# Kernel optimization log

Measured on AMD Instinct MI355X. Metric: run time of the kernel, lower is better.

Reference implementation:

```python
import jax, jax.numpy as jnp
import numpy as np

EPS = 1e-5

def conv2d(x, w, pad):
    # x: NCHW, w: OIHW, stride 1, symmetric padding
    return jax.lax.conv_general_dilated(
        x, w, window_strides=(1, 1), padding=[(pad, pad), (pad, pad)],
        dimension_numbers=('NCHW', 'OIHW', 'NCHW'))

def bn_eval(x, gamma, beta, mean, var):
    # eval-mode BatchNorm2d: per-channel affine with running stats
    s = gamma / jnp.sqrt(var + EPS)
    return x * s[None, :, None, None] + (beta - mean * s)[None, :, None, None]

def setup_inputs() -> dict:
    key = jax.random.key(0)
    ks = jax.random.split(key, 12)
    B, Cin, C, H, W = 2, 6, 64, 512, 512
    R, K = 4, 5                 # res_num, ksize
    Cf = 2 * 3 * K              # ch_out_final = 30
    d = {}
    d['feature_map'] = jax.random.normal(ks[0], (B, Cin, H, W), jnp.float32)
    d['base'] = jax.random.normal(ks[1], (B, 3, H, W), jnp.float32)
    d['w_first'] = jax.random.normal(ks[2], (C, Cin, 7, 7), jnp.float32) * 0.05
    d['kb_w1'] = jax.random.normal(ks[3], (R, C, C, 3, 3), jnp.float32) * 0.05
    d['kb_g1'] = jnp.ones((R, C), jnp.float32)
    d['kb_b1'] = jnp.zeros((R, C), jnp.float32)
    d['kb_m1'] = jax.random.normal(ks[4], (R, C), jnp.float32) * 0.1
    d['kb_v1'] = jax.random.uniform(ks[5], (R, C), jnp.float32) + 0.5
    d['kb_w2'] = jax.random.normal(ks[6], (R, C, C, 3, 3), jnp.float32) * 0.05
    d['kb_g2'] = jnp.ones((R, C), jnp.float32)
    d['kb_b2'] = jnp.zeros((R, C), jnp.float32)
    d['kb_m2'] = jax.random.normal(ks[7], (R, C), jnp.float32) * 0.1
    d['kb_v2'] = jax.random.uniform(ks[8], (R, C), jnp.float32) + 0.5
    d['w_last'] = jax.random.normal(ks[9], (Cf, C, 3, 3), jnp.float32) * 0.05
    return d

def reference(feature_map, base, w_first, kb_w1, kb_g1, kb_b1, kb_m1, kb_v1,
              kb_w2, kb_g2, kb_b2, kb_m2, kb_v2, w_last):
    K = 5
    P = K // 2
    b, _, h, w = base.shape
    # conv_first: 7x7 conv + ReLU
    y = jax.nn.relu(conv2d(feature_map, w_first, 3))
    # residual KB blocks: (conv3x3 -> BN -> ReLU) x2 + skip
    R = kb_w1.shape[0]
    for i in range(R):
        t = jax.nn.relu(bn_eval(conv2d(y, kb_w1[i], 1), kb_g1[i], kb_b1[i], kb_m1[i], kb_v1[i]))
        t = jax.nn.relu(bn_eval(conv2d(t, kb_w2[i], 1), kb_g2[i], kb_b2[i], kb_m2[i], kb_v2[i]))
        y = t + y
    # conv_last: [b, 2*3*K, h, w]
    y = conv2d(y, w_last, 1)
    Cf = y.shape[1]
    # [b,3,2K,h,w] -> [b,3,h,w,2K]
    weight = y.reshape(b, 3, Cf // 3, h, w).transpose(0, 1, 3, 4, 2)
    weight_h = jax.nn.softmax(weight[..., :K], axis=-1)  # [b,3,h,w,K]
    weight_w = jax.nn.softmax(weight[..., K:], axis=-1)
    # vertical adaptive filtering: pad H by P, unfold along H
    pad_h = jnp.pad(base, ((0, 0), (0, 0), (P, P), (0, 0)))
    unf_h = jnp.stack([pad_h[:, :, i:i + h, :] for i in range(K)], axis=-1)  # [b,3,h,w,K]
    filt_h = (unf_h * weight_h).sum(axis=-1)  # [b,3,h,w]
    # horizontal adaptive filtering: pad W by P, unfold along W
    pad_w = jnp.pad(filt_h, ((0, 0), (0, 0), (0, 0), (P, P)))
    unf_w = jnp.stack([pad_w[:, :, :, i:i + w] for i in range(K)], axis=-1)  # [b,3,h,w,K]
    return (unf_w * weight_w).sum(axis=-1)
```

## Files before the change

kernel.cpp:

```cpp
#include <hip/hip_runtime.h>
#include <math.h>

typedef __attribute__((ext_vector_type(8)))  short short8;
typedef __attribute__((ext_vector_type(4)))  float float4v;
typedef __attribute__((ext_vector_type(16))) float f32x16;
typedef unsigned int u32;

__device__ __forceinline__ unsigned short f2bf(float f) {
    union { float f; unsigned u; } x; x.f = f;
    unsigned r = x.u + 0x7FFFu + ((x.u >> 16) & 1u);
    return (unsigned short)(r >> 16);
}
__device__ __forceinline__ float bf2f(unsigned short u) {
    union { unsigned u; float f; } x; x.u = ((unsigned)u) << 16;
    return x.f;
}

__device__ __forceinline__ void gload16(const void* g, void* l) {
    __builtin_amdgcn_global_load_lds(
        (const __attribute__((address_space(1))) u32*)g,
        (__attribute__((address_space(3))) u32*)l, 16, 0, 0);
}

#define HWSZ ((size_t)512 * 512)

__global__ __launch_bounds__(256)
void prep7_k(const float* __restrict__ in, unsigned short* __restrict__ hi,
             unsigned short* __restrict__ lo)
{
    const int idx = blockIdx.x * 256 + threadIdx.x;
    const int b = idx >> 18, rem = idx & 262143;
    const int h = rem >> 9, w = rem & 511;
    unsigned short vh[8], vl[8];
#pragma unroll
    for (int c = 0; c < 8; ++c) {
        float x = (c < 6) ? in[((size_t)(b * 6 + c)) * HWSZ + (h << 9) + w] : 0.f;
        unsigned short h16 = f2bf(x);
        vh[c] = h16;
        vl[c] = f2bf(x - bf2f(h16));
    }
    const size_t o = ((size_t)idx) * 8;
    *(uint4*)(hi + o) = *(uint4*)vh;
    *(uint4*)(lo + o) = *(uint4*)vl;
}

__global__ __launch_bounds__(256)
void repack7_k(const float* __restrict__ wsrc, unsigned short* __restrict__ dhi,
               unsigned short* __restrict__ dlo)
{
    const int t = blockIdx.x * 256 + threadIdx.x;
    if (t >= 26624) return;
    const int j = t & 7, l = (t >> 3) & 63, ct = (t >> 9) & 3, kk = t >> 11;
    const int co = ct * 16 + (l & 15);
    const int s = kk * 4 + (l >> 4);
    float v = 0.f;
    if (s < 49 && j < 6)
        v = wsrc[((size_t)(co * 6 + j) * 7 + s / 7) * 7 + s % 7];
    unsigned short h16 = f2bf(v);
    dhi[t] = h16;
    dlo[t] = f2bf(v - bf2f(h16));
}

__global__ __launch_bounds__(256)
void conv7_mfma(const unsigned short* __restrict__ inhi,
                const unsigned short* __restrict__ inlo,
                const unsigned short* __restrict__ whi,
                const unsigned short* __restrict__ wlo,
                unsigned short* __restrict__ out)
{
    extern __shared__ char p_lds[];

    const int id = blockIdx.x;
    const int lid = (id & 7) * 256 + (id >> 3);
    const int w0 = (lid & 3) * 128;
    const int rest = lid >> 2;
    const int h0 = (rest & 255) * 2;
    const int b  = rest >> 8;

    const int tid = threadIdx.x;
    const int wv = tid >> 6, l = tid & 63, lq = l >> 4, lr = l & 15;

    for (int idx = tid; idx < 2144; idx += 256) {
        const int plane = idx >= 1072;
        const int rc = plane ? idx - 1072 : idx;
        const int r = rc / 134, c = rc % 134;
        const int hh = h0 - 3 + r, wc = w0 - 3 + c;
        int4 v = make_int4(0, 0, 0, 0);
        if (hh >= 0 && hh < 512 && wc >= 0 && wc < 512) {
            const unsigned short* src = plane ? inlo : inhi;
            v = *(const int4*)(src + ((((size_t)b * 512 + hh) * 512) + wc) * 8);
        }
        *(int4*)(p_lds + (size_t)idx * 16) = v;
    }
    __syncthreads();

    float4v acc[2][2][4];
#pragma unroll
    for (int pr = 0; pr < 2; ++pr)
#pragma unroll
        for (int pb = 0; pb < 2; ++pb)
#pragma unroll
            for (int ct = 0; ct < 4; ++ct)
                acc[pr][pb][ct] = (float4v){0.f, 0.f, 0.f, 0.f};

    const int cbase = wv * 32 + lr;
#pragma unroll
    for (int kk = 0; kk < 13; ++kk) {
        int s = kk * 4 + lq;
        if (s > 48) s = 48;
        const int dh = s / 7, dwd = s % 7;
        short8 ah[2][2], al[2][2];
#pragma unroll
        for (int pr = 0; pr < 2; ++pr)
#pragma unroll
            for (int pb = 0; pb < 2; ++pb) {
                const int off = ((pr + dh) * 134 + cbase + pb * 16 + dwd) * 16;
                ah[pr][pb] = *(const short8*)(p_lds + off);
                al[pr][pb] = *(const short8*)(p_lds + 17152 + off);
            }
#pragma unroll
        for (int ct = 0; ct < 4; ++ct) {
            const short8 bh = *(const short8*)(whi + ((size_t)(kk * 4 + ct) * 64 + l) * 8);
            const short8 bl = *(const short8*)(wlo + ((size_t)(kk * 4 + ct) * 64 + l) * 8);
#pragma unroll
            for (int pr = 0; pr < 2; ++pr)
#pragma unroll
                for (int pb = 0; pb < 2; ++pb) {
                    acc[pr][pb][ct] = __builtin_amdgcn_mfma_f32_16x16x32_bf16(ah[pr][pb], bh, acc[pr][pb][ct], 0, 0, 0);
                    acc[pr][pb][ct] = __builtin_amdgcn_mfma_f32_16x16x32_bf16(al[pr][pb], bh, acc[pr][pb][ct], 0, 0, 0);
                    acc[pr][pb][ct] = __builtin_amdgcn_mfma_f32_16x16x32_bf16(ah[pr][pb], bl, acc[pr][pb][ct], 0, 0, 0);
                }
        }
    }

#pragma unroll
    for (int pr = 0; pr < 2; ++pr) {
        const int h = h0 + pr;
#pragma unroll
        for (int pb = 0; pb < 2; ++pb) {
            const int col0 = w0 + wv * 32 + pb * 16 + lq * 4;
#pragma unroll
            for (int ct = 0; ct < 4; ++ct) {
                const int half = ct >> 1, colocal = (ct & 1) * 16 + lr;
#pragma unroll
                for (int rg = 0; rg < 4; ++rg) {
                    const size_t o = ((((size_t)(b * 2 + half) * 512 + h) * 512) + (col0 + rg)) * 32 + colocal;
                    out[o] = f2bf(fmaxf(acc[pr][pb][ct][rg], 0.f));
                }
            }
        }
    }
}

__global__ __launch_bounds__(256)
void repack3n_k(const float* __restrict__ w1, const float* __restrict__ w2,
                const float* __restrict__ g1, const float* __restrict__ v1,
                const float* __restrict__ g2, const float* __restrict__ v2,
                unsigned short* __restrict__ dst)
{
    const int conv = blockIdx.z;
    const float* src = (conv < 4) ? (w1 + (size_t)conv * 36864) : (w2 + (size_t)(conv - 4) * 36864);
    const float* g = (conv < 4) ? (g1 + conv * 64) : (g2 + (conv - 4) * 64);
    const float* vv = (conv < 4) ? (v1 + conv * 64) : (v2 + (conv - 4) * 64);
    unsigned short* d = dst + (size_t)conv * 36864;

    const int t = blockIdx.x * 256 + threadIdx.x;
    const int j = t & 7, l = (t >> 3) & 63;
    const int rest = t >> 9;
    const int s = rest % 9, m = rest / 9;
    const int ch = m & 1, q = m >> 1;
    const int co = ch * 32 + (l & 31);
    const int ci = q * 16 + (l >> 5) * 8 + j;
    const float sc = g[co] * rsqrtf(vv[co] + 1e-5f);
    d[t] = f2bf(src[((size_t)co * 64 + ci) * 9 + s] * sc);
}

__global__ __launch_bounds__(256)
void bias8_k(const float* __restrict__ g1, const float* __restrict__ b1,
             const float* __restrict__ m1, const float* __restrict__ v1,
             const float* __restrict__ g2, const float* __restrict__ b2,
             const float* __restrict__ m2, const float* __restrict__ v2,
             float* __restrict__ bias)
{
    const int t = blockIdx.x * 256 + threadIdx.x;
    if (t >= 512) return;
    const int conv = t >> 6, co = t & 63;
    const float* g = (conv < 4) ? (g1 + conv * 64) : (g2 + (conv - 4) * 64);
    const float* be = (conv < 4) ? (b1 + conv * 64) : (b2 + (conv - 4) * 64);
    const float* mn = (conv < 4) ? (m1 + conv * 64) : (m2 + (conv - 4) * 64);
    const float* vv = (conv < 4) ? (v1 + conv * 64) : (v2 + (conv - 4) * 64);
    const float sc = g[co] * rsqrtf(vv[co] + 1e-5f);
    bias[t] = be[co] - mn[co] * sc;
}

template <bool ADD_>
__global__ __launch_bounds__(512)
void conv3_mfma32(const unsigned short* __restrict__ in,
                  const unsigned short* __restrict__ wrp,
                  const float* __restrict__ bias,
                  const unsigned short* __restrict__ skip,
                  unsigned short* __restrict__ out)
{
    extern __shared__ char smem[];
    char* w_lds = smem;
    char* p_lds = smem + 18432;

    const int id = blockIdx.x;
    const int lid = (id & 7) * 128 + (id >> 3);
    const int w0 = (lid & 3) * 128;
    const int h0 = ((lid >> 2) & 127) * 4;
    const int b  = lid >> 9;

    const int tid = threadIdx.x;
    const int wv = tid >> 6, l = tid & 63;
    const int rw = wv >> 1, tq = wv & 1;
    const int lo5 = l & 31, hi = l >> 5;

    f32x16 acc[2][2];
#pragma unroll
    for (int ch = 0; ch < 2; ++ch)
#pragma unroll
        for (int t4 = 0; t4 < 2; ++t4)
#pragma unroll
            for (int e = 0; e < 16; ++e) acc[ch][t4][e] = 0.f;

    for (int q = 0; q < 4; ++q) {
        if (q) __syncthreads();

        const unsigned short* wq  = wrp + (size_t)q * 9216;
        const unsigned short* inp = in + (size_t)(b * 2 + (q >> 1)) * HWSZ * 32;
        const int cb8 = (q & 1) * 2;

        for (int i = wv; i < 42; i += 8) {
            if (i < 18) {
                gload16(wq + (size_t)i * 512 + l * 8, w_lds + (size_t)i * 1024);
            } else {
                const int j2 = i - 18, p = j2 >> 1, half = j2 & 1;
                const int row = p >> 1, kg = p & 1;
                const int hh = h0 - 1 + row;
                if (hh >= 0 && hh < 512)
                    gload16(inp + ((size_t)hh * 512 + w0 + half * 64 + l) * 32 + (cb8 + kg) * 8,
                            p_lds + (size_t)(p * 132 + 1 + half * 64) * 16);
            }
        }
        if (tid < 24) {
            const int p = tid >> 1, side = tid & 1;
            const int row = p >> 1, kg = p & 1;
            const int hh = h0 - 1 + row;
            const int wc = side ? (w0 + 128) : (w0 - 1);
            int4 v = make_int4(0, 0, 0, 0);
            if (hh >= 0 && hh < 512 && wc >= 0 && wc < 512)
                v = *(const int4*)(inp + ((size_t)hh * 512 + wc) * 32 + (cb8 + kg) * 8);
            *(int4*)(p_lds + (size_t)(p * 132 + (side ? 129 : 0)) * 16) = v;
        }
        if (h0 == 0) {
            for (int g = tid; g < 264; g += 512)
                *(int4*)(p_lds + (size_t)g * 16) = make_int4(0, 0, 0, 0);
        } else if (h0 == 508) {
            for (int g = tid; g < 264; g += 512)
                *(int4*)(p_lds + (size_t)(10 * 132 + g) * 16) = make_int4(0, 0, 0, 0);
        }
        __syncthreads();

#pragma unroll
        for (int s = 0; s < 9; ++s) {
            const int dh = s / 3, dwd = s % 3;
            const int row = rw + dh;
            short8 pf[2];
#pragma unroll
            for (int t4 = 0; t4 < 2; ++t4) {
                const int px = tq * 64 + t4 * 32 + dwd + lo5;
                pf[t4] = *(const short8*)(p_lds +
                    ((size_t)((row * 2 + hi) * 132 + px)) * 16);
            }
#pragma unroll
            for (int ch = 0; ch < 2; ++ch) {
                const short8 w8 = *(const short8*)(w_lds +
                    ((size_t)((ch * 9 + s) * 64 + l)) * 16);
#pragma unroll
                for (int t4 = 0; t4 < 2; ++t4)
                    acc[ch][t4] = __builtin_amdgcn_mfma_f32_32x32x16_bf16(
                        pf[t4], w8, acc[ch][t4], 0, 0, 0);
            }
        }
    }

    const int h = h0 + rw;
#pragma unroll
    for (int ch = 0; ch < 2; ++ch) {
        const float bvs = bias[ch * 32 + lo5];
        const size_t pbase = ((size_t)(b * 2 + ch) * HWSZ + (size_t)h * 512);
#pragma unroll
        for (int t4 = 0; t4 < 2; ++t4) {
#pragma unroll
            for (int reg = 0; reg < 16; ++reg) {
                const int pxl = tq * 64 + t4 * 32 + (reg & 3) + 8 * (reg >> 2) + 4 * hi;
                const size_t o = (pbase + (w0 + pxl)) * 32 + lo5;
                float v = fmaxf(acc[ch][t4][reg] + bvs, 0.f);
                if (ADD_) v += bf2f(skip[o]);
                out[o] = f2bf(v);
            }
        }
    }
}

__global__ __launch_bounds__(256)
void repackL_k(const float* __restrict__ wsrc, unsigned short* __restrict__ d)
{
    const int t = blockIdx.x * 256 + threadIdx.x;
    const int j = t & 7, l = (t >> 3) & 63, ct = (t >> 9) & 1, kks = t >> 10;
    const int hf = kks / 9, s = kks % 9;
    const int co = ct * 16 + (l & 15);
    const int ci = hf * 32 + (l >> 4) * 8 + j;
    d[t] = (co < 30) ? f2bf(wsrc[((size_t)co * 64 + ci) * 9 + s]) : (unsigned short)0;
}

template <int NCOT, int OC>
__global__ __launch_bounds__(256)
void conv3_last(const unsigned short* __restrict__ in,
                const unsigned short* __restrict__ wrp,
                unsigned short* __restrict__ out)
{
    extern __shared__ char smem[];
    unsigned short* w_lds = (unsigned short*)smem;
    char* p_lds = smem + NCOT * 9 * 1024;

    const int id = blockIdx.x;
    const int lid = (id & 7) * 256 + (id >> 3);
    const int w0 = (lid & 3) * 128;
    const int rest = lid >> 2;
    const int h0 = (rest & 255) * 2;
    const int b  = rest >> 8;

    const int tid = threadIdx.x;
    const int wv = tid >> 6, l = tid & 63, lq = l >> 4, lr = l & 15;
    const int cbase = wv * 32 + lr;

    float4v acc[2][2][NCOT];
#pragma unroll
    for (int pr = 0; pr < 2; ++pr)
#pragma unroll
        for (int pb = 0; pb < 2; ++pb)
#pragma unroll
            for (int ct = 0; ct < NCOT; ++ct)
                acc[pr][pb][ct] = (float4v){0.f, 0.f, 0.f, 0.f};

    for (int ph = 0; ph < 2; ++ph) {
        const int4* wsrc = (const int4*)(wrp + (size_t)ph * 9 * NCOT * 512);
        for (int i = tid; i < NCOT * 9 * 64; i += 256)
            ((int4*)w_lds)[i] = wsrc[i];
        const unsigned short* inp = in + (size_t)(b * 2 + ph) * HWSZ * 32;
        for (int idx = tid; idx < 2080; idx += 256) {
            const int G = idx & 3, c = (idx >> 2) % 130, rr = idx / 520;
            const int hh = h0 - 1 + rr, wc = w0 - 1 + c;
            int4 v = make_int4(0, 0, 0, 0);
            if (hh >= 0 && hh < 512 && wc >= 0 && wc < 512)
                v = *(const int4*)(inp + ((size_t)hh * 512 + wc) * 32 + G * 8);
            *(int4*)(p_lds + ((size_t)(G * 521 + rr * 130 + c)) * 16) = v;
        }
        __syncthreads();

#pragma unroll
        for (int s = 0; s < 9; ++s) {
            const int dh = s / 3, dwd = s % 3;
            short8 a[2][2];
#pragma unroll
            for (int pr = 0; pr < 2; ++pr)
#pragma unroll
                for (int pb = 0; pb < 2; ++pb)
                    a[pr][pb] = *(const short8*)(p_lds +
                        ((size_t)(lq * 521 + (pr + dh) * 130 + cbase + pb * 16 + dwd)) * 16);
#pragma unroll
            for (int ct = 0; ct < NCOT; ++ct) {
                const short8 bw = *(const short8*)(w_lds + ((size_t)(s * NCOT + ct) * 64 + l) * 8);
#pragma unroll
                for (int pr = 0; pr < 2; ++pr)
#pragma unroll
                    for (int pb = 0; pb < 2; ++pb)
                        acc[pr][pb][ct] = __builtin_amdgcn_mfma_f32_16x16x32_bf16(
                            a[pr][pb], bw, acc[pr][pb][ct], 0, 0, 0);
            }
        }
        __syncthreads();
    }

#pragma unroll
    for (int pr = 0; pr < 2; ++pr) {
        const int h = h0 + pr;
#pragma unroll
        for (int pb = 0; pb < 2; ++pb) {
            const int col0 = w0 + wv * 32 + pb * 16 + lq * 4;
#pragma unroll
            for (int ct = 0; ct < NCOT; ++ct) {
                const int co = ct * 16 + lr;
                if (co < OC) {
#pragma unroll
                    for (int rg = 0; rg < 4; ++rg) {
                        const size_t o = (((size_t)(b * OC + co) * 512 + h) * 512) + (col0 + rg);
                        out[o] = f2bf(acc[pr][pb][ct][rg]);
                    }
                }
            }
        }
    }
}

__global__ __launch_bounds__(256)
void filt_fused_k(const unsigned short* __restrict__ wl, const float* __restrict__ base,
                  float* __restrict__ out)
{
    __shared__ float F[516];

    const int id = blockIdx.x;
    const int lid = (id & 7) * 384 + (id >> 3);
    const int h = lid & 511;
    const int bc = lid >> 9;
    const int b = bc / 3, c = bc % 3;
    const int t = threadIdx.x;

    if (t < 2) F[t] = 0.f;
    if (t >= 254) F[t + 260] = 0.f;

    const size_t rowoff = (size_t)h * 512;
    const unsigned short* wv_p = wl + ((size_t)(b * 30 + c * 10) * HWSZ) + rowoff;
    const unsigned short* wh_p = wv_p + 5 * HWSZ;
    const float* bp = base + (size_t)bc * HWSZ;

#pragma unroll
    for (int wi = 0; wi < 2; ++wi) {
        const int w = t + wi * 256;
        float v[5]; float mx = -1e30f;
#pragma unroll
        for (int i = 0; i < 5; ++i) { v[i] = bf2f(wv_p[(size_t)i * HWSZ + w]); mx = fmaxf(mx, v[i]); }
        float sm = 0.f;
#pragma unroll
        for (int i = 0; i < 5; ++i) { v[i] = __expf(v[i] - mx); sm += v[i]; }
        const float inv = 1.f / sm;
        float acc = 0.f;
#pragma unroll
        for (int i = 0; i < 5; ++i) {
            const int hh = h + i - 2;
            const float bvv = (hh >= 0 && hh < 512) ? bp[(size_t)hh * 512 + w] : 0.f;
            acc = fmaf(bvv, v[i] * inv, acc);
        }
        F[w + 2] = acc;
    }
    __syncthreads();

#pragma unroll
    for (int wi = 0; wi < 2; ++wi) {
        const int w = t + wi * 256;
        float v[5]; float mx = -1e30f;
#pragma unroll
        for (int i = 0; i < 5; ++i) { v[i] = bf2f(wh_p[(size_t)i * HWSZ + w]); mx = fmaxf(mx, v[i]); }
        float sm = 0.f;
#pragma unroll
        for (int i = 0; i < 5; ++i) { v[i] = __expf(v[i] - mx); sm += v[i]; }
        const float inv = 1.f / sm;
        float acc = 0.f;
#pragma unroll
        for (int i = 0; i < 5; ++i)
            acc = fmaf(F[w + i], v[i] * inv, acc);
        out[(size_t)bc * HWSZ + rowoff + w] = acc;
    }
}

extern "C" void kernel_launch(void* const* d_in, const int* in_sizes, int n_in,
                              void* d_out, int out_size, void* d_ws, size_t ws_size,
                              hipStream_t stream)
{
    const float* fm      = (const float*)d_in[0];
    const float* base    = (const float*)d_in[1];
    const float* w_first = (const float*)d_in[2];
    const float* kb_w1   = (const float*)d_in[3];
    const float* kb_g1   = (const float*)d_in[4];
    const float* kb_b1   = (const float*)d_in[5];
    const float* kb_m1   = (const float*)d_in[6];
    const float* kb_v1   = (const float*)d_in[7];
    const float* kb_w2   = (const float*)d_in[8];
    const float* kb_g2   = (const float*)d_in[9];
    const float* kb_b2   = (const float*)d_in[10];
    const float* kb_m2   = (const float*)d_in[11];
    const float* kb_v2   = (const float*)d_in[12];
    const float* w_last  = (const float*)d_in[13];

    char* ws = (char*)d_ws;
    unsigned short* wrp3n  = (unsigned short*)ws;
    unsigned short* wrpL   = wrp3n + (size_t)8 * 36864;
    unsigned short* wrp7hi = wrpL + 18432;
    unsigned short* wrp7lo = wrp7hi + 26624;
    float*          biasws = (float*)(wrp7lo + 26624);
    unsigned short* actA = (unsigned short*)(ws + (1 << 20));
    unsigned short* actB = actA + (size_t)2 * HWSZ * 64;
    unsigned short* actC = actB + (size_t)2 * HWSZ * 64;
    unsigned short* in7hi = actB;
    unsigned short* in7lo = actB + (size_t)2 * HWSZ * 8;
    unsigned short* logits = actC;

    hipFuncSetAttribute((const void*)conv3_mfma32<false>,
                        hipFuncAttributeMaxDynamicSharedMemorySize, 43776);
    hipFuncSetAttribute((const void*)conv3_mfma32<true>,
                        hipFuncAttributeMaxDynamicSharedMemorySize, 43776);
    hipFuncSetAttribute((const void*)conv3_last<2, 30>,
                        hipFuncAttributeMaxDynamicSharedMemorySize, 51776);
    hipFuncSetAttribute((const void*)conv7_mfma,
                        hipFuncAttributeMaxDynamicSharedMemorySize, 34304);

    dim3 blk(256);

    repack3n_k<<<dim3(144, 1, 8), blk, 0, stream>>>(kb_w1, kb_w2, kb_g1, kb_v1, kb_g2, kb_v2, wrp3n);
    bias8_k<<<dim3(2, 1, 1), blk, 0, stream>>>(kb_g1, kb_b1, kb_m1, kb_v1, kb_g2, kb_b2, kb_m2, kb_v2, biasws);
    repackL_k<<<dim3(72, 1, 1), blk, 0, stream>>>(w_last, wrpL);
    repack7_k<<<dim3(104, 1, 1), blk, 0, stream>>>(w_first, wrp7hi, wrp7lo);
    prep7_k<<<dim3(2048, 1, 1), blk, 0, stream>>>(fm, in7hi, in7lo);

    conv7_mfma<<<dim3(2048, 1, 1), blk, 34304, stream>>>(in7hi, in7lo, wrp7hi, wrp7lo, actA);

    unsigned short* cur = actA;
    unsigned short* oth = actC;
    for (int i = 0; i < 4; ++i) {
        conv3_mfma32<false><<<dim3(1024, 1, 1), dim3(512), 43776, stream>>>(
            cur, wrp3n + (size_t)i * 36864, biasws + i * 64, nullptr, actB);
        conv3_mfma32<true><<<dim3(1024, 1, 1), dim3(512), 43776, stream>>>(
            actB, wrp3n + (size_t)(4 + i) * 36864, biasws + (4 + i) * 64, cur, oth);
        unsigned short* t = cur; cur = oth; oth = t;
    }

    conv3_last<2, 30><<<dim3(2048, 1, 1), blk, 51776, stream>>>(cur, wrpL, logits);

    filt_fused_k<<<dim3(3072, 1, 1), blk, 0, stream>>>(logits, base, (float*)d_out);
}
```

Baseline: 552.5 us.

## Rewrite last conv with 32x32x16 MFMA, weight-stationary tiling and async LDS loads

Replaces the final 64->30 3x3 conv kernel with one that uses 32x32x16 bf16 MFMA, putting the 32 padded output channels on the A side and pixels on the B side. The weight repack layout changes to match. All weights are loaded once via global_load_lds, and the input tile is staged in four channel-quarter passes using direct-to-LDS loads plus explicit halo and boundary zeroing. The aim is fewer MFMA issues, less register-level shuffling and cheaper LDS staging, at the cost of more barriers and more shared memory per block.

```diff
diff --git a/kernel.cpp b/kernel.cpp
--- a/kernel.cpp
+++ b/kernel.cpp
@@ -305,102 +305,103 @@
 }
 
 __global__ __launch_bounds__(256)
-void repackL_k(const float* __restrict__ wsrc, unsigned short* __restrict__ d)
+void repackLn_k(const float* __restrict__ wsrc, unsigned short* __restrict__ d)
 {
     const int t = blockIdx.x * 256 + threadIdx.x;
-    const int j = t & 7, l = (t >> 3) & 63, ct = (t >> 9) & 1, kks = t >> 10;
-    const int hf = kks / 9, s = kks % 9;
-    const int co = ct * 16 + (l & 15);
-    const int ci = hf * 32 + (l >> 4) * 8 + j;
+    const int j = t & 7, l = (t >> 3) & 63;
+    const int rest = t >> 9;
+    const int s = rest % 9, q = rest / 9;
+    const int co = l & 31;
+    const int ci = q * 16 + (l >> 5) * 8 + j;
     d[t] = (co < 30) ? f2bf(wsrc[((size_t)co * 64 + ci) * 9 + s]) : (unsigned short)0;
 }
 
-template <int NCOT, int OC>
-__global__ __launch_bounds__(256)
-void conv3_last(const unsigned short* __restrict__ in,
+__global__ __launch_bounds__(256)
+void conv_lastN(const unsigned short* __restrict__ in,
                 const unsigned short* __restrict__ wrp,
                 unsigned short* __restrict__ out)
 {
     extern __shared__ char smem[];
-    unsigned short* w_lds = (unsigned short*)smem;
-    char* p_lds = smem + NCOT * 9 * 1024;
+    char* w_lds = smem;
+    char* p_lds = smem + 36864;
 
     const int id = blockIdx.x;
     const int lid = (id & 7) * 256 + (id >> 3);
     const int w0 = (lid & 3) * 128;
-    const int rest = lid >> 2;
-    const int h0 = (rest & 255) * 2;
-    const int b  = rest >> 8;
+    const int h0 = ((lid >> 2) & 255) * 2;
+    const int b  = lid >> 10;
 
     const int tid = threadIdx.x;
-    const int wv = tid >> 6, l = tid & 63, lq = l >> 4, lr = l & 15;
-    const int cbase = wv * 32 + lr;
-
-    float4v acc[2][2][NCOT];
-#pragma unroll
-    for (int pr = 0; pr < 2; ++pr)
-#pragma unroll
-        for (int pb = 0; pb < 2; ++pb)
-#pragma unroll
-            for (int ct = 0; ct < NCOT; ++ct)
-                acc[pr][pb][ct] = (float4v){0.f, 0.f, 0.f, 0.f};
-
-    for (int ph = 0; ph < 2; ++ph) {
-        const int4* wsrc = (const int4*)(wrp + (size_t)ph * 9 * NCOT * 512);
-        for (int i = tid; i < NCOT * 9 * 64; i += 256)
-            ((int4*)w_lds)[i] = wsrc[i];
-        const unsigned short* inp = in + (size_t)(b * 2 + ph) * HWSZ * 32;
-        for (int idx = tid; idx < 2080; idx += 256) {
-            const int G = idx & 3, c = (idx >> 2) % 130, rr = idx / 520;
-            const int hh = h0 - 1 + rr, wc = w0 - 1 + c;
+    const int wv = tid >> 6, l = tid & 63;
+    const int rw = wv >> 1, tq = wv & 1;
+    const int lo5 = l & 31, hi = l >> 5;
+
+    f32x16 acc[2];
+#pragma unroll
+    for (int t4 = 0; t4 < 2; ++t4)
+#pragma unroll
+        for (int e = 0; e < 16; ++e) acc[t4][e] = 0.f;
+
+    for (int q = 0; q < 4; ++q) {
+        if (q) __syncthreads();
+
+        const unsigned short* inp = in + (size_t)(b * 2 + (q >> 1)) * HWSZ * 32;
+        const int cb8 = (q & 1) * 2;
+
+        if (q == 0)
+            for (int i = wv; i < 36; i += 4)
+                gload16(wrp + (size_t)i * 512 + l * 8, w_lds + (size_t)i * 1024);
+        for (int i = wv; i < 16; i += 4) {
+            const int p = i >> 1, half = i & 1;
+            const int row = p >> 1, kg = p & 1;
+            const int hh = h0 - 1 + row;
+            if (hh >= 0 && hh < 512)
+                gload16(inp + ((size_t)hh * 512 + w0 + half * 64 + l) * 32 + (cb8 + kg) * 8,
+                        p_lds + (size_t)(p * 132 + 1 + half * 64) * 16);
+        }
+        if (tid < 16) {
+            const int p = tid >> 1, side = tid & 1;
+            const int row = p >> 1, kg = p & 1;
+            const int hh = h0 - 1 + row;
+            const int wc = side ? (w0 + 128) : (w0 - 1);
             int4 v = make_int4(0, 0, 0, 0);
             if (hh >= 0 && hh < 512 && wc >= 0 && wc < 512)
-                v = *(const int4*)(inp + ((size_t)hh * 512 + wc) * 32 + G * 8);
-            *(int4*)(p_lds + ((size_t)(G * 521 + rr * 130 + c)) * 16) = v;
+                v = *(const int4*)(inp + ((size_t)hh * 512 + wc) * 32 + (cb8 + kg) * 8);
+            *(int4*)(p_lds + (size_t)(p * 132 + (side ? 129 : 0)) * 16) = v;
+        }
+        if (h0 == 0) {
+            for (int g = tid; g < 264; g += 256)
+                *(int4*)(p_lds + (size_t)g * 16) = make_int4(0, 0, 0, 0);
+        } else if (h0 == 510) {
+            for (int g = tid; g < 264; g += 256)
+                *(int4*)(p_lds + (size_t)(6 * 132 + g) * 16) = make_int4(0, 0, 0, 0);
         }
         __syncthreads();
 
 #pragma unroll
         for (int s = 0; s < 9; ++s) {
             const int dh = s / 3, dwd = s % 3;
-            short8 a[2][2];
-#pragma unroll
-            for (int pr = 0; pr < 2; ++pr)
-#pragma unroll
-                for (int pb = 0; pb < 2; ++pb)
-                    a[pr][pb] = *(const short8*)(p_lds +
-                        ((size_t)(lq * 521 + (pr + dh) * 130 + cbase + pb * 16 + dwd)) * 16);
-#pragma unroll
-            for (int ct = 0; ct < NCOT; ++ct) {
-                const short8 bw = *(const short8*)(w_lds + ((size_t)(s * NCOT + ct) * 64 + l) * 8);
-#pragma unroll
-                for (int pr = 0; pr < 2; ++pr)
-#pragma unroll
-                    for (int pb = 0; pb < 2; ++pb)
-                        acc[pr][pb][ct] = __builtin_amdgcn_mfma_f32_16x16x32_bf16(
-                            a[pr][pb], bw, acc[pr][pb][ct], 0, 0, 0);
-            }
-        }
-        __syncthreads();
-    }
-
-#pragma unroll
-    for (int pr = 0; pr < 2; ++pr) {
-        const int h = h0 + pr;
-#pragma unroll
-        for (int pb = 0; pb < 2; ++pb) {
-            const int col0 = w0 + wv * 32 + pb * 16 + lq * 4;
-#pragma unroll
-            for (int ct = 0; ct < NCOT; ++ct) {
-                const int co = ct * 16 + lr;
-                if (co < OC) {
-#pragma unroll
-                    for (int rg = 0; rg < 4; ++rg) {
-                        const size_t o = (((size_t)(b * OC + co) * 512 + h) * 512) + (col0 + rg);
-                        out[o] = f2bf(acc[pr][pb][ct][rg]);
-                    }
-                }
-            }
+            const int row = rw + dh;
+            const short8 wf = *(const short8*)(w_lds + ((size_t)((q * 9 + s) * 64 + l)) * 16);
+#pragma unroll
+            for (int t4 = 0; t4 < 2; ++t4) {
+                const int px = tq * 64 + t4 * 32 + dwd + lo5;
+                const short8 pf = *(const short8*)(p_lds +
+                    ((size_t)((row * 2 + hi) * 132 + px)) * 16);
+                acc[t4] = __builtin_amdgcn_mfma_f32_32x32x16_bf16(wf, pf, acc[t4], 0, 0, 0);
+            }
+        }
+    }
+
+    const int h = h0 + rw;
+#pragma unroll
+    for (int t4 = 0; t4 < 2; ++t4) {
+        const int px = w0 + tq * 64 + t4 * 32 + lo5;
+#pragma unroll
+        for (int reg = 0; reg < 16; ++reg) {
+            const int co = (reg & 3) + 8 * (reg >> 2) + 4 * hi;
+            if (co < 30)
+                out[(((size_t)(b * 30 + co) * 512 + h) * 512) + px] = f2bf(acc[t4][reg]);
         }
     }
 }
@@ -501,8 +502,8 @@
                         hipFuncAttributeMaxDynamicSharedMemorySize, 43776);
     hipFuncSetAttribute((const void*)conv3_mfma32<true>,
                         hipFuncAttributeMaxDynamicSharedMemorySize, 43776);
-    hipFuncSetAttribute((const void*)conv3_last<2, 30>,
-                        hipFuncAttributeMaxDynamicSharedMemorySize, 51776);
+    hipFuncSetAttribute((const void*)conv_lastN,
+                        hipFuncAttributeMaxDynamicSharedMemorySize, 53760);
     hipFuncSetAttribute((const void*)conv7_mfma,
                         hipFuncAttributeMaxDynamicSharedMemorySize, 34304);
 
@@ -510,7 +511,7 @@
 
     repack3n_k<<<dim3(144, 1, 8), blk, 0, stream>>>(kb_w1, kb_w2, kb_g1, kb_v1, kb_g2, kb_v2, wrp3n);
     bias8_k<<<dim3(2, 1, 1), blk, 0, stream>>>(kb_g1, kb_b1, kb_m1, kb_v1, kb_g2, kb_b2, kb_m2, kb_v2, biasws);
-    repackL_k<<<dim3(72, 1, 1), blk, 0, stream>>>(w_last, wrpL);
+    repackLn_k<<<dim3(72, 1, 1), blk, 0, stream>>>(w_last, wrpL);
     repack7_k<<<dim3(104, 1, 1), blk, 0, stream>>>(w_first, wrp7hi, wrp7lo);
     prep7_k<<<dim3(2048, 1, 1), blk, 0, stream>>>(fm, in7hi, in7lo);
 
@@ -526,7 +527,7 @@
         unsigned short* t = cur; cur = oth; oth = t;
     }
 
-    conv3_last<2, 30><<<dim3(2048, 1, 1), blk, 51776, stream>>>(cur, wrpL, logits);
+    conv_lastN<<<dim3(2048, 1, 1), blk, 53760, stream>>>(cur, wrpL, logits);
 
     filt_fused_k<<<dim3(3072, 1, 1), blk, 0, stream>>>(logits, base, (float*)d_out);
 }
```

New measurement: 540.9 us, median of 2. 2.1% less time.
